# Kernel tuning notes

Hardware: AMD Instinct MI355X
Metric: run time of the kernel (lower is better)

The kernel has to match this reference:

```python
import jax, jax.numpy as jnp
import numpy as np

NU, NM, D, E = 100000, 20000, 128, 1000000


def _seg_mean(feats, idx, n):
    # scatter-mean: zero for nodes with no incoming edges (PyG semantics)
    s = jax.ops.segment_sum(feats, idx, num_segments=n)
    c = jax.ops.segment_sum(jnp.ones((idx.shape[0], 1), feats.dtype), idx, num_segments=n)
    return s / jnp.maximum(c, 1.0)


def _hetero_sage(xu, xm, e_src, e_dst, Wl_um, Wr_um, b_um, Wl_mu, Wr_mu, b_mu):
    # ('user','rates','movie'): aggregate user features at movies
    agg_m = _seg_mean(xu[e_src], e_dst, xm.shape[0])          # [Nm, D]
    out_m = agg_m @ Wl_um + b_um + xm @ Wr_um                  # [Nm, H]
    # ('movie','rev_rates','user'): aggregate movie features at users
    agg_u = _seg_mean(xm[e_dst], e_src, xu.shape[0])          # [Nu, D]
    out_u = agg_u @ Wl_mu + b_mu + xu @ Wr_mu                  # [Nu, H]
    return out_u, out_m


def setup_inputs() -> dict:
    key = jax.random.key(0)
    ks = jax.random.split(key, 20)
    glorot = lambda k: (jax.random.normal(k, (D, D), jnp.float32) / np.sqrt(D)).astype(jnp.float32)
    inp = {
        "x_user": jax.random.normal(ks[0], (NU, D), jnp.float32),
        "x_movie": jax.random.normal(ks[1], (NM, D), jnp.float32),
        "edge_src": jax.random.randint(ks[2], (E,), 0, NU),
        "edge_dst": jax.random.randint(ks[3], (E,), 0, NM),
    }
    names = ["Wl1_um", "Wr1_um", "Wl1_mu", "Wr1_mu", "Wl2_um", "Wr2_um", "Wl2_mu", "Wr2_mu"]
    for i, n in enumerate(names):
        inp[n] = glorot(ks[4 + i])
    inp["b1_um"] = jnp.zeros((D,), jnp.float32)
    inp["b1_mu"] = jnp.zeros((D,), jnp.float32)
    inp["b2_um"] = jnp.zeros((D,), jnp.float32)
    inp["b2_mu"] = jnp.zeros((D,), jnp.float32)
    return inp


def reference(x_user, x_movie, Wl1_um, Wr1_um, Wl1_mu, Wr1_mu, Wl2_um, Wr2_um, Wl2_mu, Wr2_mu, b1_um, b1_mu, b2_um, b2_mu, edge_src, edge_dst):
    # layer 1 + relu (dropout = identity in eval) + residual
    h1_u, h1_m = _hetero_sage(x_user, x_movie, edge_src, edge_dst,
                              Wl1_um, Wr1_um, b1_um, Wl1_mu, Wr1_mu, b1_mu)
    r_u = x_user + jax.nn.relu(h1_u)
    r_m = x_movie + jax.nn.relu(h1_m)
    # layer 2 (dropout = identity in eval)
    out_u, out_m = _hetero_sage(r_u, r_m, edge_src, edge_dst,
                                Wl2_um, Wr2_um, b2_um, Wl2_mu, Wr2_mu, b2_mu)
    return out_u, out_m
```

## Files before the change

kernel.cpp:

```cpp
#include <hip/hip_runtime.h>
#include <stdint.h>

typedef unsigned short u16;
typedef unsigned int u32;
typedef __attribute__((ext_vector_type(8))) short short8;
typedef __attribute__((ext_vector_type(4))) float f32x4;
typedef __attribute__((ext_vector_type(4))) u32 u32x4;

__device__ __forceinline__ u16 f2bf(float f) {
    u32 x = __float_as_uint(f);
    u32 r = x + 0x7FFFu + ((x >> 16) & 1u);
    return (u16)(r >> 16);
}
__device__ __forceinline__ u32 pack2bf(float a, float b) {
    return (u32)f2bf(a) | ((u32)f2bf(b) << 16);
}
__device__ __forceinline__ float bflo(u32 w) { return __uint_as_float(w << 16); }
__device__ __forceinline__ float bfhi(u32 w) { return __uint_as_float(w & 0xFFFF0000u); }

struct WPtrs {
    const float* wl[4];
    const float* wr[4];
    u16* wout[4];
};

__global__ __launch_bounds__(256)
void prep_kernel(const int* __restrict__ src, const int* __restrict__ dst,
                 int* __restrict__ cnt, int* __restrict__ ranku,
                 int* __restrict__ rankm, int E, int nu, int nm,
                 const float* __restrict__ xu, const float* __restrict__ xm,
                 u32* __restrict__ xub, u32* __restrict__ xmb,
                 int eg4, int cg, WPtrs wp) {
    const int bid = blockIdx.x;
    const int tid = threadIdx.x;
    if (bid < eg4) {
        const int e0 = bid * 1024 + tid;
        int sv[4], dv[4];
        bool ok[4];
#pragma unroll
        for (int k = 0; k < 4; ++k) {
            int e = e0 + k * 256;
            ok[k] = (e < E);
            if (ok[k]) { sv[k] = src[e]; dv[k] = dst[e]; }
        }
#pragma unroll
        for (int k = 0; k < 4; ++k) {
            int e = e0 + k * 256;
            if (ok[k]) {
                if ((unsigned)sv[k] < (unsigned)nu &&
                    (unsigned)dv[k] < (unsigned)nm) {
                    ranku[e] = atomicAdd(&cnt[sv[k]], 1);
                    rankm[e] = atomicAdd(&cnt[nu + dv[k]], 1);
                } else {
                    ranku[e] = -1;
                }
            }
        }
    } else if (bid < eg4 + cg) {
        const int id = (bid - eg4) * 1024 + tid * 4;
        const int nuc = nu * 64;
        const int tot = nuc + nm * 64;
        if (id < tot) {
            const float* fin;
            u32* fout;
            int rel;
            if (id < nuc) { fin = xu; fout = xub; rel = id; }
            else          { fin = xm; fout = xmb; rel = id - nuc; }
            float4 p0 = ((const float4*)fin)[(rel >> 1)];
            float4 p1 = ((const float4*)fin)[(rel >> 1) + 1];
            u32x4 o = { pack2bf(p0.x, p0.y), pack2bf(p0.z, p0.w),
                        pack2bf(p1.x, p1.y), pack2bf(p1.z, p1.w) };
            *(u32x4*)(fout + rel) = o;
        }
    } else {
        const int unit = (bid - eg4 - cg) * 4 + (tid >> 6);
        if (unit < 256) {
            const int stack = unit >> 6, r = unit & 63, t = r >> 3, s = r & 7;
            const int lane = tid & 63;
            const float* Wl = wp.wl[stack];
            const float* Wr = wp.wr[stack];
            u16* outw = wp.wout[stack];
            const int n = t * 16 + (lane & 15);
            const int k0 = s * 32 + (lane >> 4) * 8;
            u16 v[8];
#pragma unroll
            for (int j = 0; j < 8; ++j) {
                int k = k0 + j;
                float f = (k < 128) ? Wl[k * 128 + n] : Wr[(k - 128) * 128 + n];
                v[j] = f2bf(f);
            }
            *(short8*)(outw + ((size_t)(t * 8 + s) * 64 + lane) * 8) = *(short8*)v;
        }
    }
}

__global__ __launch_bounds__(256)
void scan_partial(const int* __restrict__ cnt, int* __restrict__ bsum, int n) {
    __shared__ int s[256];
    const int tid = threadIdx.x;
    int base = blockIdx.x * 4096 + tid * 16;
    int sum = 0;
#pragma unroll
    for (int k = 0; k < 16; ++k) {
        int i = base + k;
        if (i < n) sum += cnt[i];
    }
    s[tid] = sum;
    __syncthreads();
    for (int d = 128; d > 0; d >>= 1) {
        if (tid < d) s[tid] += s[tid + d];
        __syncthreads();
    }
    if (tid == 0) bsum[blockIdx.x] = s[0];
}

__global__ __launch_bounds__(256)
void scan_apply(const int* __restrict__ cnt, const int* __restrict__ bsum,
                int* __restrict__ off, int n, int nb) {
    __shared__ int s[256];
    __shared__ int sb[64];
    __shared__ int pfx;
    const int tid = threadIdx.x;
    int base = blockIdx.x * 4096 + tid * 16;
    int v[16];
    int sum = 0;
#pragma unroll
    for (int k = 0; k < 16; ++k) {
        int i = base + k;
        v[k] = (i < n) ? cnt[i] : 0;
        sum += v[k];
    }
    s[tid] = sum;
    if (tid < 64) sb[tid] = (tid < nb) ? bsum[tid] : 0;
    __syncthreads();
    for (int d = 1; d < 256; d <<= 1) {
        int t = (tid >= d) ? s[tid - d] : 0;
        __syncthreads();
        s[tid] += t;
        __syncthreads();
    }
    if (tid == 0) {
        int p = 0;
        for (int b2 = 0; b2 < (int)blockIdx.x; ++b2) p += sb[b2];
        pfx = p;
        if ((int)blockIdx.x == nb - 1) off[n] = p + s[255];
    }
    __syncthreads();
    int run = pfx + s[tid] - sum;
#pragma unroll
    for (int k = 0; k < 16; ++k) {
        int i = base + k;
        if (i < n) off[i] = run;
        run += v[k];
    }
}

__global__ __launch_bounds__(256)
void fill_pos(const int* __restrict__ src, const int* __restrict__ dst,
              const int* __restrict__ ranku, const int* __restrict__ rankm,
              const int* __restrict__ off, int* __restrict__ nbr,
              int E, int nu) {
    const int e0 = blockIdx.x * 1024 + threadIdx.x;
    int sv[4], dv[4], ru[4], rm[4];
#pragma unroll
    for (int k = 0; k < 4; ++k) {
        int e = e0 + k * 256;
        ru[k] = -1;
        if (e < E) {
            ru[k] = ranku[e];
            sv[k] = src[e]; dv[k] = dst[e]; rm[k] = rankm[e];
        }
    }
#pragma unroll
    for (int k = 0; k < 4; ++k) {
        if (ru[k] >= 0) {
            nbr[off[sv[k]] + ru[k]] = dv[k];
            nbr[off[nu + dv[k]] + rm[k]] = sv[k];
        }
    }
}

template <int L1>
__device__ __forceinline__ void fused_body(
    const u32* __restrict__ featb, const float* __restrict__ xf,
    const u32* __restrict__ xb, const int* __restrict__ off,
    const int* __restrict__ nbr, const u16* __restrict__ wt,
    const float* __restrict__ bias, void* __restrict__ outp, int N, int blk) {
    __shared__ u32 sVb[32][132];
    const int tid = threadIdx.x;
    const int lane = tid & 63;
    const int wave = tid >> 6;
    const int base = blk * 32;
    const int q = lane >> 4;
    const int cl = lane & 15;

    for (int c = 0; c < 8; ++c) {
        const int i = wave * 8 + c;
        const int n = base + i;
        if (n < N) {
            const int b = off[n], e = off[n + 1];
            float a0 = 0.f, a1 = 0.f, a2 = 0.f, a3 = 0.f;
            float a4 = 0.f, a5 = 0.f, a6 = 0.f, a7 = 0.f;
            int t = b;
            if (t + 31 < e) {
                int g[8];
#pragma unroll
                for (int k = 0; k < 8; ++k) g[k] = nbr[t + 4 * k + q];
                while (t + 63 < e) {
                    int gn[8];
#pragma unroll
                    for (int k = 0; k < 8; ++k) gn[k] = nbr[t + 32 + 4 * k + q];
#pragma unroll
                    for (int k = 0; k < 8; ++k) {
                        u32x4 v = *(const u32x4*)(featb + (size_t)g[k] * 64 + cl * 4);
                        a0 += bflo(v.x); a1 += bfhi(v.x);
                        a2 += bflo(v.y); a3 += bfhi(v.y);
                        a4 += bflo(v.z); a5 += bfhi(v.z);
                        a6 += bflo(v.w); a7 += bfhi(v.w);
                    }
#pragma unroll
                    for (int k = 0; k < 8; ++k) g[k] = gn[k];
                    t += 32;
                }
#pragma unroll
                for (int k = 0; k < 8; ++k) {
                    u32x4 v = *(const u32x4*)(featb + (size_t)g[k] * 64 + cl * 4);
                    a0 += bflo(v.x); a1 += bfhi(v.x);
                    a2 += bflo(v.y); a3 += bfhi(v.y);
                    a4 += bflo(v.z); a5 += bfhi(v.z);
                    a6 += bflo(v.w); a7 += bfhi(v.w);
                }
                t += 32;
            }
            for (; t < e; t += 4) {
                int it = t + q;
                if (it < e) {
                    u32x4 v = *(const u32x4*)(featb + (size_t)nbr[it] * 64 + cl * 4);
                    a0 += bflo(v.x); a1 += bfhi(v.x);
                    a2 += bflo(v.y); a3 += bfhi(v.y);
                    a4 += bflo(v.z); a5 += bfhi(v.z);
                    a6 += bflo(v.w); a7 += bfhi(v.w);
                }
            }
            a0 += __shfl_xor(a0, 16); a0 += __shfl_xor(a0, 32);
            a1 += __shfl_xor(a1, 16); a1 += __shfl_xor(a1, 32);
            a2 += __shfl_xor(a2, 16); a2 += __shfl_xor(a2, 32);
            a3 += __shfl_xor(a3, 16); a3 += __shfl_xor(a3, 32);
            a4 += __shfl_xor(a4, 16); a4 += __shfl_xor(a4, 32);
            a5 += __shfl_xor(a5, 16); a5 += __shfl_xor(a5, 32);
            a6 += __shfl_xor(a6, 16); a6 += __shfl_xor(a6, 32);
            a7 += __shfl_xor(a7, 16); a7 += __shfl_xor(a7, 32);
            const int dg = e - b;
            const float inv = 1.0f / (float)(dg > 1 ? dg : 1);
            if (q == 0) {
                u32x4 o = { pack2bf(a0 * inv, a1 * inv), pack2bf(a2 * inv, a3 * inv),
                            pack2bf(a4 * inv, a5 * inv), pack2bf(a6 * inv, a7 * inv) };
                *(u32x4*)&sVb[i][cl * 4] = o;
            }
            if (L1) {
                const float2 xv = ((const float2*)xf)[(size_t)n * 64 + lane];
                sVb[i][64 + lane] = pack2bf(xv.x, xv.y);
            } else {
                sVb[i][64 + lane] = xb[(size_t)n * 64 + lane];
            }
        } else {
            sVb[i][lane] = 0u;
            sVb[i][64 + lane] = 0u;
        }
    }
    __syncthreads();

    const int t0 = wave * 2, t1 = t0 + 1;
    const u16* sVbu = (const u16*)sVb;
    const short8* wtp = (const short8*)wt;

    f32x4 acc00 = {0.f, 0.f, 0.f, 0.f};
    f32x4 acc01 = {0.f, 0.f, 0.f, 0.f};
    f32x4 acc10 = {0.f, 0.f, 0.f, 0.f};
    f32x4 acc11 = {0.f, 0.f, 0.f, 0.f};
#pragma unroll
    for (int s = 0; s < 8; ++s) {
        short8 a0 = *(const short8*)(sVbu + (size_t)cl * 264 + s * 32 + q * 8);
        short8 a1 = *(const short8*)(sVbu + (size_t)(16 + cl) * 264 + s * 32 + q * 8);
        short8 b0 = wtp[(size_t)(t0 * 8 + s) * 64 + lane];
        short8 b1 = wtp[(size_t)(t1 * 8 + s) * 64 + lane];
        acc00 = __builtin_amdgcn_mfma_f32_16x16x32_bf16(a0, b0, acc00, 0, 0, 0);
        acc01 = __builtin_amdgcn_mfma_f32_16x16x32_bf16(a0, b1, acc01, 0, 0, 0);
        acc10 = __builtin_amdgcn_mfma_f32_16x16x32_bf16(a1, b0, acc10, 0, 0, 0);
        acc11 = __builtin_amdgcn_mfma_f32_16x16x32_bf16(a1, b1, acc11, 0, 0, 0);
    }

    const int n0 = t0 * 16 + cl, n1 = t1 * 16 + cl;
    const float bj0 = bias[n0], bj1 = bias[n1];
#pragma unroll
    for (int mt = 0; mt < 2; ++mt) {
        const f32x4& c0 = mt ? acc10 : acc00;
        const f32x4& c1 = mt ? acc11 : acc01;
#pragma unroll
        for (int r = 0; r < 4; ++r) {
            const int m = mt * 16 + q * 4 + r;
            const int node = base + m;
            if (node < N) {
                float h0 = c0[r] + bj0;
                float h1 = c1[r] + bj1;
                if (L1) {
                    u16* ob = (u16*)outp;
                    float x0 = xf[(size_t)node * 128 + n0];
                    float x1 = xf[(size_t)node * 128 + n1];
                    ob[(size_t)node * 128 + n0] = f2bf(x0 + fmaxf(h0, 0.f));
                    ob[(size_t)node * 128 + n1] = f2bf(x1 + fmaxf(h1, 0.f));
                } else {
                    float* o = (float*)outp;
                    o[(size_t)node * 128 + n0] = h0;
                    o[(size_t)node * 128 + n1] = h1;
                }
            }
        }
    }
}

__global__ __launch_bounds__(256)
void fused_l1(const u32* __restrict__ featb, const float* __restrict__ xf,
              const int* __restrict__ off, const int* __restrict__ nbr,
              const u16* __restrict__ wt, const float* __restrict__ bias,
              void* __restrict__ outp, int N) {
    fused_body<1>(featb, xf, nullptr, off, nbr, wt, bias, outp, N, blockIdx.x);
}

__global__ __launch_bounds__(256)
void fused_l2_dual(const u32* __restrict__ Abf, const u32* __restrict__ rmb,
                   const int* __restrict__ off, const int* __restrict__ nbr,
                   const u16* __restrict__ wtm, const u16* __restrict__ wtu,
                   const float* __restrict__ bm, const float* __restrict__ bu,
                   float* __restrict__ outm, float* __restrict__ outu,
                   int nm, int nu, int gm) {
    if ((int)blockIdx.x < gm)
        fused_body<0>(Abf, nullptr, rmb, off + nu, nbr, wtm, bm, outm, nm,
                      blockIdx.x);
    else
        fused_body<0>(rmb, nullptr, Abf, off, nbr, wtu, bu, outu, nu,
                      blockIdx.x - gm);
}

extern "C" void kernel_launch(void* const* d_in, const int* in_sizes, int n_in,
                              void* d_out, int out_size, void* d_ws, size_t ws_size,
                              hipStream_t stream) {
    const int nu = in_sizes[0] / 128;
    const int nm = in_sizes[1] / 128;
    const int E = in_sizes[2];

    const float* xu = (const float*)d_in[0];
    const float* xm = (const float*)d_in[1];
    const int* esrc = (const int*)d_in[2];
    const int* edst = (const int*)d_in[3];
    const float* Wl1_um = (const float*)d_in[4];
    const float* Wr1_um = (const float*)d_in[5];
    const float* Wl1_mu = (const float*)d_in[6];
    const float* Wr1_mu = (const float*)d_in[7];
    const float* Wl2_um = (const float*)d_in[8];
    const float* Wr2_um = (const float*)d_in[9];
    const float* Wl2_mu = (const float*)d_in[10];
    const float* Wr2_mu = (const float*)d_in[11];
    const float* b1_um = (const float*)d_in[12];
    const float* b1_mu = (const float*)d_in[13];
    const float* b2_um = (const float*)d_in[14];
    const float* b2_mu = (const float*)d_in[15];

    float* out_u = (float*)d_out;
    float* out_m = out_u + (size_t)nu * 128;

    const int ntot = nu + nm;
    const int NB = (ntot + 4095) / 4096;
    int* cnt = (int*)d_ws;
    int* off = cnt + ntot;
    int* bsum = off + ntot + 1;
    int* ranku = bsum + ((NB + 15) & ~15);
    int* rankm = ranku + E;
    int* nbr = rankm + E;
    size_t int_bytes = (size_t)((nbr + 2 * (size_t)E) - (int*)d_ws) * 4;
    size_t wt_off = (int_bytes + 63) & ~(size_t)63;
    u16* wt1_um = (u16*)((char*)d_ws + wt_off);
    u16* wt1_mu = wt1_um + 32768;
    u16* wt2_um = wt1_mu + 32768;
    u16* wt2_mu = wt2_um + 32768;
    u32* Abf = (u32*)((char*)d_ws + wt_off + 4 * 65536);
    u32* xmb = Abf + (size_t)nu * 64;
    u32* rmb = xmb + (size_t)nm * 64;

    const int eg4 = (E + 1023) / 1024;
    const int cg = ((nu + nm) * 64 + 1023) / 1024;

    WPtrs wp;
    wp.wl[0] = Wl1_um; wp.wr[0] = Wr1_um; wp.wout[0] = wt1_um;
    wp.wl[1] = Wl1_mu; wp.wr[1] = Wr1_mu; wp.wout[1] = wt1_mu;
    wp.wl[2] = Wl2_um; wp.wr[2] = Wr2_um; wp.wout[2] = wt2_um;
    wp.wl[3] = Wl2_mu; wp.wr[3] = Wr2_mu; wp.wout[3] = wt2_mu;

    hipMemsetAsync(cnt, 0, (size_t)ntot * 4, stream);
    prep_kernel<<<eg4 + cg + 64, 256, 0, stream>>>(
        esrc, edst, cnt, ranku, rankm, E, nu, nm, xu, xm, Abf, xmb, eg4, cg, wp);
    scan_partial<<<NB, 256, 0, stream>>>(cnt, bsum, ntot);
    scan_apply<<<NB, 256, 0, stream>>>(cnt, bsum, off, ntot, NB);
    fill_pos<<<eg4, 256, 0, stream>>>(esrc, edst, ranku, rankm, off, nbr, E, nu);

    const int gm = (nm + 31) / 32;
    const int gu = (nu + 31) / 32;

    fused_l1<<<gm, 256, 0, stream>>>(Abf, xm, off + nu, nbr, wt1_um, b1_um,
                                     rmb, nm);
    fused_l1<<<gu, 256, 0, stream>>>(xmb, xu, off, nbr, wt1_mu, b1_mu,
                                     Abf, nu);

    fused_l2_dual<<<gm + gu, 256, 0, stream>>>(
        Abf, rmb, off, nbr, wt2_um, wt2_mu, b2_um, b2_mu, out_m, out_u,
        nm, nu, gm);
}
```

Baseline: 572.9 us.

## Shrink fused SAGE blocks to 16 nodes and simplify neighbor gather loop

Halves the per-block node tile from 32 to 16 and the block size from 256 to 128 threads, with launch bounds asking for 8 resident blocks per SIMD. The MFMA stage now has each wave compute four output column tiles for a single 16-row tile instead of a 2x2 tile arrangement. The neighbor gather replaces the 32-edge software-pipelined loop with a simpler 16-edge unrolled loop, so lower-degree nodes also use the unrolled path. The aim is more blocks and better occupancy and load balance on the irregular gather. The cost is that weight tiles are fetched twice as often per node and index prefetching across iterations is lost.

```diff
diff --git a/kernel.cpp b/kernel.cpp
--- a/kernel.cpp
+++ b/kernel.cpp
@@ -186,11 +186,11 @@
     const u32* __restrict__ xb, const int* __restrict__ off,
     const int* __restrict__ nbr, const u16* __restrict__ wt,
     const float* __restrict__ bias, void* __restrict__ outp, int N, int blk) {
-    __shared__ u32 sVb[32][132];
+    __shared__ u32 sVb[16][132];
     const int tid = threadIdx.x;
     const int lane = tid & 63;
     const int wave = tid >> 6;
-    const int base = blk * 32;
+    const int base = blk * 16;
     const int q = lane >> 4;
     const int cl = lane & 15;
 
@@ -202,44 +202,30 @@
             float a0 = 0.f, a1 = 0.f, a2 = 0.f, a3 = 0.f;
             float a4 = 0.f, a5 = 0.f, a6 = 0.f, a7 = 0.f;
             int t = b;
-            if (t + 31 < e) {
-                int g[8];
-#pragma unroll
-                for (int k = 0; k < 8; ++k) g[k] = nbr[t + 4 * k + q];
-                while (t + 63 < e) {
-                    int gn[8];
-#pragma unroll
-                    for (int k = 0; k < 8; ++k) gn[k] = nbr[t + 32 + 4 * k + q];
-#pragma unroll
-                    for (int k = 0; k < 8; ++k) {
-                        u32x4 v = *(const u32x4*)(featb + (size_t)g[k] * 64 + cl * 4);
-                        a0 += bflo(v.x); a1 += bfhi(v.x);
-                        a2 += bflo(v.y); a3 += bfhi(v.y);
-                        a4 += bflo(v.z); a5 += bfhi(v.z);
-                        a6 += bflo(v.w); a7 += bfhi(v.w);
-                    }
-#pragma unroll
-                    for (int k = 0; k < 8; ++k) g[k] = gn[k];
-                    t += 32;
-                }
-#pragma unroll
-                for (int k = 0; k < 8; ++k) {
-                    u32x4 v = *(const u32x4*)(featb + (size_t)g[k] * 64 + cl * 4);
-                    a0 += bflo(v.x); a1 += bfhi(v.x);
-                    a2 += bflo(v.y); a3 += bfhi(v.y);
-                    a4 += bflo(v.z); a5 += bfhi(v.z);
-                    a6 += bflo(v.w); a7 += bfhi(v.w);
-                }
-                t += 32;
+            for (; t + 15 < e; t += 16) {
+                int g0 = nbr[t + q];
+                int g1 = nbr[t + 4 + q];
+                int g2 = nbr[t + 8 + q];
+                int g3 = nbr[t + 12 + q];
+                u32x4 v0 = *(const u32x4*)(featb + (size_t)g0 * 64 + cl * 4);
+                u32x4 v1 = *(const u32x4*)(featb + (size_t)g1 * 64 + cl * 4);
+                u32x4 v2 = *(const u32x4*)(featb + (size_t)g2 * 64 + cl * 4);
+                u32x4 v3 = *(const u32x4*)(featb + (size_t)g3 * 64 + cl * 4);
+                a0 += bflo(v0.x); a1 += bfhi(v0.x); a2 += bflo(v0.y); a3 += bfhi(v0.y);
+                a4 += bflo(v0.z); a5 += bfhi(v0.z); a6 += bflo(v0.w); a7 += bfhi(v0.w);
+                a0 += bflo(v1.x); a1 += bfhi(v1.x); a2 += bflo(v1.y); a3 += bfhi(v1.y);
+                a4 += bflo(v1.z); a5 += bfhi(v1.z); a6 += bflo(v1.w); a7 += bfhi(v1.w);
+                a0 += bflo(v2.x); a1 += bfhi(v2.x); a2 += bflo(v2.y); a3 += bfhi(v2.y);
+                a4 += bflo(v2.z); a5 += bfhi(v2.z); a6 += bflo(v2.w); a7 += bfhi(v2.w);
+                a0 += bflo(v3.x); a1 += bfhi(v3.x); a2 += bflo(v3.y); a3 += bfhi(v3.y);
+                a4 += bflo(v3.z); a5 += bfhi(v3.z); a6 += bflo(v3.w); a7 += bfhi(v3.w);
             }
             for (; t < e; t += 4) {
                 int it = t + q;
                 if (it < e) {
                     u32x4 v = *(const u32x4*)(featb + (size_t)nbr[it] * 64 + cl * 4);
-                    a0 += bflo(v.x); a1 += bfhi(v.x);
-                    a2 += bflo(v.y); a3 += bfhi(v.y);
-                    a4 += bflo(v.z); a5 += bfhi(v.z);
-                    a6 += bflo(v.w); a7 += bfhi(v.w);
+                    a0 += bflo(v.x); a1 += bfhi(v.x); a2 += bflo(v.y); a3 += bfhi(v.y);
+                    a4 += bflo(v.z); a5 += bfhi(v.z); a6 += bflo(v.w); a7 += bfhi(v.w);
                 }
             }
             a0 += __shfl_xor(a0, 16); a0 += __shfl_xor(a0, 32);
@@ -270,56 +256,52 @@
     }
     __syncthreads();
 
-    const int t0 = wave * 2, t1 = t0 + 1;
+    const int t0 = wave * 4;
     const u16* sVbu = (const u16*)sVb;
     const short8* wtp = (const short8*)wt;
 
-    f32x4 acc00 = {0.f, 0.f, 0.f, 0.f};
-    f32x4 acc01 = {0.f, 0.f, 0.f, 0.f};
-    f32x4 acc10 = {0.f, 0.f, 0.f, 0.f};
-    f32x4 acc11 = {0.f, 0.f, 0.f, 0.f};
+    f32x4 acc0 = {0.f, 0.f, 0.f, 0.f};
+    f32x4 acc1 = {0.f, 0.f, 0.f, 0.f};
+    f32x4 acc2 = {0.f, 0.f, 0.f, 0.f};
+    f32x4 acc3 = {0.f, 0.f, 0.f, 0.f};
 #pragma unroll
     for (int s = 0; s < 8; ++s) {
-        short8 a0 = *(const short8*)(sVbu + (size_t)cl * 264 + s * 32 + q * 8);
-        short8 a1 = *(const short8*)(sVbu + (size_t)(16 + cl) * 264 + s * 32 + q * 8);
-        short8 b0 = wtp[(size_t)(t0 * 8 + s) * 64 + lane];
-        short8 b1 = wtp[(size_t)(t1 * 8 + s) * 64 + lane];
-        acc00 = __builtin_amdgcn_mfma_f32_16x16x32_bf16(a0, b0, acc00, 0, 0, 0);
-        acc01 = __builtin_amdgcn_mfma_f32_16x16x32_bf16(a0, b1, acc01, 0, 0, 0);
-        acc10 = __builtin_amdgcn_mfma_f32_16x16x32_bf16(a1, b0, acc10, 0, 0, 0);
-        acc11 = __builtin_amdgcn_mfma_f32_16x16x32_bf16(a1, b1, acc11, 0, 0, 0);
-    }
-
-    const int n0 = t0 * 16 + cl, n1 = t1 * 16 + cl;
-    const float bj0 = bias[n0], bj1 = bias[n1];
-#pragma unroll
-    for (int mt = 0; mt < 2; ++mt) {
-        const f32x4& c0 = mt ? acc10 : acc00;
-        const f32x4& c1 = mt ? acc11 : acc01;
+        short8 a = *(const short8*)(sVbu + (size_t)cl * 264 + s * 32 + q * 8);
+        short8 b0 = wtp[(size_t)((t0 + 0) * 8 + s) * 64 + lane];
+        short8 b1 = wtp[(size_t)((t0 + 1) * 8 + s) * 64 + lane];
+        short8 b2 = wtp[(size_t)((t0 + 2) * 8 + s) * 64 + lane];
+        short8 b3 = wtp[(size_t)((t0 + 3) * 8 + s) * 64 + lane];
+        acc0 = __builtin_amdgcn_mfma_f32_16x16x32_bf16(a, b0, acc0, 0, 0, 0);
+        acc1 = __builtin_amdgcn_mfma_f32_16x16x32_bf16(a, b1, acc1, 0, 0, 0);
+        acc2 = __builtin_amdgcn_mfma_f32_16x16x32_bf16(a, b2, acc2, 0, 0, 0);
+        acc3 = __builtin_amdgcn_mfma_f32_16x16x32_bf16(a, b3, acc3, 0, 0, 0);
+    }
+
+#pragma unroll
+    for (int tt = 0; tt < 4; ++tt) {
+        const f32x4& cc = tt == 0 ? acc0 : tt == 1 ? acc1 : tt == 2 ? acc2 : acc3;
+        const int nn = (t0 + tt) * 16 + cl;
+        const float bj = bias[nn];
 #pragma unroll
         for (int r = 0; r < 4; ++r) {
-            const int m = mt * 16 + q * 4 + r;
+            const int m = q * 4 + r;
             const int node = base + m;
             if (node < N) {
-                float h0 = c0[r] + bj0;
-                float h1 = c1[r] + bj1;
+                float h = cc[r] + bj;
                 if (L1) {
                     u16* ob = (u16*)outp;
-                    float x0 = xf[(size_t)node * 128 + n0];
-                    float x1 = xf[(size_t)node * 128 + n1];
-                    ob[(size_t)node * 128 + n0] = f2bf(x0 + fmaxf(h0, 0.f));
-                    ob[(size_t)node * 128 + n1] = f2bf(x1 + fmaxf(h1, 0.f));
+                    float x0 = xf[(size_t)node * 128 + nn];
+                    ob[(size_t)node * 128 + nn] = f2bf(x0 + fmaxf(h, 0.f));
                 } else {
                     float* o = (float*)outp;
-                    o[(size_t)node * 128 + n0] = h0;
-                    o[(size_t)node * 128 + n1] = h1;
+                    o[(size_t)node * 128 + nn] = h;
                 }
             }
         }
     }
 }
 
-__global__ __launch_bounds__(256)
+__global__ __launch_bounds__(128, 8)
 void fused_l1(const u32* __restrict__ featb, const float* __restrict__ xf,
               const int* __restrict__ off, const int* __restrict__ nbr,
               const u16* __restrict__ wt, const float* __restrict__ bias,
@@ -327,7 +309,7 @@
     fused_body<1>(featb, xf, nullptr, off, nbr, wt, bias, outp, N, blockIdx.x);
 }
 
-__global__ __launch_bounds__(256)
+__global__ __launch_bounds__(128, 8)
 void fused_l2_dual(const u32* __restrict__ Abf, const u32* __restrict__ rmb,
                    const int* __restrict__ off, const int* __restrict__ nbr,
                    const u16* __restrict__ wtm, const u16* __restrict__ wtu,
@@ -403,15 +385,15 @@
     scan_apply<<<NB, 256, 0, stream>>>(cnt, bsum, off, ntot, NB);
     fill_pos<<<eg4, 256, 0, stream>>>(esrc, edst, ranku, rankm, off, nbr, E, nu);
 
-    const int gm = (nm + 31) / 32;
-    const int gu = (nu + 31) / 32;
-
-    fused_l1<<<gm, 256, 0, stream>>>(Abf, xm, off + nu, nbr, wt1_um, b1_um,
+    const int gm = (nm + 15) / 16;
+    const int gu = (nu + 15) / 16;
+
+    fused_l1<<<gm, 128, 0, stream>>>(Abf, xm, off + nu, nbr, wt1_um, b1_um,
                                      rmb, nm);
-    fused_l1<<<gu, 256, 0, stream>>>(xmb, xu, off, nbr, wt1_mu, b1_mu,
+    fused_l1<<<gu, 128, 0, stream>>>(xmb, xu, off, nbr, wt1_mu, b1_mu,
                                      Abf, nu);
 
-    fused_l2_dual<<<gm + gu, 256, 0, stream>>>(
+    fused_l2_dual<<<gm + gu, 128, 0, stream>>>(
         Abf, rmb, off, nbr, wt2_um, wt2_mu, b2_um, b2_mu, out_m, out_u,
         nm, nu, gm);
 }
```

Result: faster. 513.9 us (-10.3%).
